# Optimization experiments

Measured on AMD Instinct MI355X. Metric: run time of the kernel, lower is better.

## Reference

```python
import jax, jax.numpy as jnp
import numpy as np
import math


def pos_enc_3d(h, w, d, c):
    # Faithful PositionalEncoding3D: channels = ceil(c/6)*2 (made even), sin/cos per axis.
    cpe = int(np.ceil(c / 6) * 2)
    if cpe % 2:
        cpe += 1
    inv_freq = 1.0 / (10000.0 ** (np.arange(0, cpe, 2, dtype=np.float32) / cpe))

    def axis_emb(n):
        s = np.arange(n, dtype=np.float32)[:, None] * inv_freq  # (n, cpe//2)
        return np.concatenate([np.sin(s), np.cos(s)], axis=-1)  # (n, cpe)

    ex = np.broadcast_to(axis_emb(h)[:, None, None, :], (h, w, d, cpe))
    ey = np.broadcast_to(axis_emb(w)[None, :, None, :], (h, w, d, cpe))
    ez = np.broadcast_to(axis_emb(d)[None, None, :, :], (h, w, d, cpe))
    emb = np.concatenate([ex, ey, ez], axis=-1)[..., :c]  # (h,w,d,c)
    return jnp.asarray(np.transpose(emb, (3, 0, 1, 2)))  # (c,h,w,d)


def conv3d(x, w, b):
    # x: (b,c,h,w,d), w: (o,i,3,3,3), padding=1
    y = jax.lax.conv_general_dilated(
        x, w, window_strides=(1, 1, 1), padding=[(1, 1)] * 3,
        dimension_numbers=('NCHWD', 'OIHWD', 'NCHWD'))
    return y + b[None, :, None, None, None]


def setup_inputs() -> dict:
    key = jax.random.key(0)
    ks = jax.random.split(key, 12)
    B, C, H, W, D = 2, 64, 16, 16, 16
    C8 = C // 8
    s_emb = 1.0 / math.sqrt(C)
    s_conv = 1.0 / math.sqrt(C * 27)
    return {
        'x': jax.random.normal(ks[0], (B, C, H, W, D), dtype=jnp.float32),
        'Wq': jax.random.normal(ks[1], (C, C), dtype=jnp.float32) * s_emb,
        'Wk': jax.random.normal(ks[2], (C, C), dtype=jnp.float32) * s_emb,
        'Wv': jax.random.normal(ks[3], (C, C), dtype=jnp.float32) * s_emb,
        'qw': jax.random.normal(ks[4], (C8, C, 3, 3, 3), dtype=jnp.float32) * s_conv,
        'qb': jax.random.normal(ks[5], (C8,), dtype=jnp.float32) * 0.01,
        'kw': jax.random.normal(ks[6], (C8, C, 3, 3, 3), dtype=jnp.float32) * s_conv,
        'kb': jax.random.normal(ks[7], (C8,), dtype=jnp.float32) * 0.01,
        'vw': jax.random.normal(ks[8], (C, C, 3, 3, 3), dtype=jnp.float32) * s_conv,
        'vb': jax.random.normal(ks[9], (C,), dtype=jnp.float32) * 0.01,
        'lam1': jax.random.normal(ks[10], (1,), dtype=jnp.float32) * 0.5,
        'lam2': jax.random.normal(ks[11], (1,), dtype=jnp.float32) * 0.5,
    }


def reference(x, Wq, Wk, Wv, qw, qb, kw, kb, vw, vb, lam1, lam2):
    b, c, h, w, d = x.shape
    n = h * w * d
    # NOTE: torch code does `x += pe` in-place inside SelfAttention, so the
    # PE-added x is also what GSA and the residual see.
    pe = pos_enc_3d(h, w, d, c)  # (c,h,w,d)
    x_pe = x + pe[None]

    # ---- SelfAttention (TSA) ----
    tok = x_pe.reshape(b, c, n).transpose(0, 2, 1)  # (b,n,c)
    Q = jnp.einsum('bnc,cd->bnd', tok, Wq)
    K = jnp.einsum('bnc,cd->bnd', tok, Wk)
    V = jnp.einsum('bnc,cd->bnd', tok, Wv)
    A = jax.nn.softmax(jnp.einsum('bic,bjc->bij', Q, K) / math.sqrt(c), axis=-1)
    tsa = jnp.einsum('bij,bjc->bic', A, V).transpose(0, 2, 1).reshape(b, c, h, w, d)

    # ---- GlobalSpatialAttention (GSA) ----
    M = conv3d(x_pe, qw, qb).reshape(b, c // 8, n)   # (b,c/8,n)
    Nk = conv3d(x_pe, kw, kb).reshape(b, c // 8, n)  # (b,c/8,n)
    Wv_ = conv3d(x_pe, vw, vb).reshape(b, c, n)      # (b,c,n)
    Bm = jax.nn.softmax(jnp.einsum('bci,bcj->bij', M, Nk), axis=-1)  # (b,n,n)
    gsa = jnp.einsum('bcj,bij->bci', Wv_, Bm).reshape(b, c, h, w, d)

    return lam1[0] * tsa + lam2[0] * gsa + x_pe
```

## Files before the change

### kernel.cpp

```cpp
#include <hip/hip_runtime.h>
#include <math.h>

#define BB 2
#define CC 64
#define NN 4096
#define CN (CC*NN)
#define NJ 8
#define NT ((NN/NJ)/64)

#define LOG2E 1.4426950408889634f
#define QSCALE 0.18033688011112042f
#define RESC_THR 8.0f

#define XT_ROWS 4097
#define WQKV_OFF (27*80*64)

typedef __attribute__((ext_vector_type(8))) short short8;
typedef __attribute__((ext_vector_type(4))) float float4v;
typedef unsigned short ushortT;

__device__ __forceinline__ ushortT f2bf(float x) {
    union { float f; unsigned u; } v; v.f = x;
    unsigned r = v.u + 0x7FFF + ((v.u >> 16) & 1);
    return (ushortT)(r >> 16);
}
__device__ __forceinline__ float bf2f(short s) {
    union { unsigned u; float f; } v;
    v.u = ((unsigned)(unsigned short)s) << 16;
    return v.f;
}
__device__ __forceinline__ unsigned pk2(float a, float b) {
    unsigned ua = __float_as_uint(a) + 0x8000u;
    unsigned ub = __float_as_uint(b) + 0x8000u;
    return __builtin_amdgcn_perm(ub, ua, 0x07060302);
}

__device__ __forceinline__ float pe_tab_val(int c, int pos) {
    int c2 = (c < 22) ? c : (c < 44) ? (c - 22) : (c - 44);
    int is_cos = (c2 >= 11);
    int k = c2 - (is_cos ? 11 : 0);
    float freq = exp2f(-1.2079738526863135f * (float)k);
    float arg = (float)pos * freq;
    return is_cos ? cosf(arg) : sinf(arg);
}

__global__ __launch_bounds__(256) void k_pre(const float* __restrict__ x,
                                             const float* __restrict__ qw,
                                             const float* __restrict__ kw,
                                             const float* __restrict__ vw,
                                             const float* __restrict__ Wq,
                                             const float* __restrict__ Wk,
                                             const float* __restrict__ Wv,
                                             float* __restrict__ xpe,
                                             ushortT* __restrict__ Xt,
                                             ushortT* __restrict__ Wr,
                                             ushortT* __restrict__ Qb,
                                             ushortT* __restrict__ Kb,
                                             ushortT* __restrict__ Vtb) {
    int blk = blockIdx.x, t = threadIdx.x;
    if (blk < 384) {
        __shared__ float sT[64][65];
        __shared__ float sPE[64][17];
        __shared__ ushortT sWt[64][72];
        __shared__ ushortT sVt[64][72];
        int mat = blk >> 7;
        int rest = blk & 127;
        int b = rest >> 6, pos0 = (rest & 63) * 64;

        #pragma unroll
        for (int k = 0; k < 4; k++) {
            int e = t + k * 256;
            int c = e >> 4, coord = e & 15;
            sPE[c][coord] = pe_tab_val(c, coord);
        }
        __syncthreads();

        int pin = t & 63, cg0 = t >> 6;
        #pragma unroll
        for (int pass = 0; pass < 16; pass++) {
            int c = pass * 4 + cg0;
            int pos = pos0 + pin;
            int coord = (c < 22) ? (pos >> 8) : (c < 44) ? ((pos >> 4) & 15) : (pos & 15);
            size_t gi = (size_t)(b * 64 + c) * NN + pos;
            float v = x[gi] + sPE[c][coord];
            if (mat == 0) xpe[gi] = v;
            sT[c][pin] = v;
        }
        {
            const float* Wm = (mat == 0) ? Wq : (mat == 1) ? Wk : Wv;
            float sc = (mat == 0) ? QSCALE : 1.f;
            #pragma unroll
            for (int p = 0; p < 4; p++) {
                int idx = t + p * 256;
                int c = idx >> 4, d4 = (idx & 15) * 4;
                float4 wv = *(const float4*)&Wm[c * 64 + d4];
                sWt[d4 + 0][c] = f2bf(wv.x * sc);
                sWt[d4 + 1][c] = f2bf(wv.y * sc);
                sWt[d4 + 2][c] = f2bf(wv.z * sc);
                sWt[d4 + 3][c] = f2bf(wv.w * sc);
            }
        }
        __syncthreads();

        if (mat == 0) {
            int po = t & 63, cg = t >> 6;
            #pragma unroll
            for (int half = 0; half < 2; half++) {
                int c0 = cg * 8 + half * 32;
                union { ushortT u[8]; short8 s; } pk_;
                #pragma unroll
                for (int e = 0; e < 8; e++) pk_.u[e] = f2bf(sT[c0 + e][po]);
                *(short8*)(Xt + ((size_t)b * XT_ROWS + pos0 + po + 1) * 64 + c0) = pk_.s;
            }
            if ((rest & 63) == 0 && t < 64)
                Xt[((size_t)b * XT_ROWS) * 64 + t] = 0;
        }

        int w = t >> 6, l = t & 63, lane15 = l & 15, q = l >> 4;
        int row = w * 16 + lane15;
        short8 a0, a1;
        {
            union { ushortT u[8]; short8 s; } t0, t1;
            #pragma unroll
            for (int e = 0; e < 8; e++) {
                t0.u[e] = f2bf(sT[q * 8 + e][row]);
                t1.u[e] = f2bf(sT[32 + q * 8 + e][row]);
            }
            a0 = t0.s; a1 = t1.s;
        }

        float4v acc[4];
        #pragma unroll
        for (int cg = 0; cg < 4; cg++) {
            const ushortT* wrow = &sWt[cg * 16 + lane15][0];
            short8 b0 = *(const short8*)(wrow + q * 8);
            short8 b1 = *(const short8*)(wrow + 32 + q * 8);
            float4v a = (float4v)0.f;
            a = __builtin_amdgcn_mfma_f32_16x16x32_bf16(a0, b0, a, 0, 0, 0);
            a = __builtin_amdgcn_mfma_f32_16x16x32_bf16(a1, b1, a, 0, 0, 0);
            acc[cg] = a;
        }
        if (mat < 2) {
            #pragma unroll
            for (int cg = 0; cg < 4; cg++)
                #pragma unroll
                for (int r = 0; r < 4; r++)
                    sVt[w * 16 + q * 4 + r][cg * 16 + lane15] = f2bf(acc[cg][r]);
            __syncthreads();
            ushortT* o = (mat == 0) ? Qb : Kb;
            int pl = t >> 2, sg = t & 3;
            short8 v0 = *(const short8*)&sVt[pl][sg * 16];
            short8 v1 = *(const short8*)&sVt[pl][sg * 16 + 8];
            size_t bq = ((size_t)(b * NN + pos0 + pl)) * 64 + sg * 16;
            *(short8*)(o + bq) = v0;
            *(short8*)(o + bq + 8) = v1;
        } else {
            #pragma unroll
            for (int cg = 0; cg < 4; cg++)
                #pragma unroll
                for (int r = 0; r < 4; r++)
                    sVt[cg * 16 + lane15][w * 16 + q * 4 + r] = f2bf(acc[cg][r]);
            __syncthreads();
            int c2 = t >> 2, seg = t & 3;
            short8 v0 = *(const short8*)&sVt[c2][seg * 16];
            short8 v1 = *(const short8*)&sVt[c2][seg * 16 + 8];
            size_t base = ((size_t)(b * 64 + c2)) * NN + pos0 + seg * 16;
            *(short8*)(Vtb + base) = v0;
            *(short8*)(Vtb + base + 8) = v1;
        }
    } else {
        int idx = (blk - 384) * 256 + t;
        if (idx < WQKV_OFF) {
            int ic = idx & 63;
            int oc = (idx >> 6) % 80;
            int tap = idx / 5120;
            float v;
            if (oc < 8)       v = qw[(oc * 64 + ic) * 27 + tap] * LOG2E;
            else if (oc < 16) v = kw[((oc - 8) * 64 + ic) * 27 + tap];
            else              v = vw[((oc - 16) * 64 + ic) * 27 + tap];
            Wr[idx] = f2bf(v);
        }
    }
}

template<int IS_TSA>
__device__ __forceinline__ void stage_load(short8* kst, short8* vst,
                                           const ushortT* __restrict__ Km,
                                           const ushortT* __restrict__ Vt,
                                           int b, int jb, int t) {
    if (IS_TSA) {
        #pragma unroll
        for (int ps = 0; ps < 2; ps++) {
            int idx = ps * 256 + t, j = idx >> 3, g = idx & 7;
            kst[ps] = *(const short8*)(Km + ((size_t)(b * NN + jb + j)) * 64 + g * 8);
        }
    } else {
        if (t < 64)
            kst[0] = *(const short8*)(Km + ((size_t)(b * NN + jb + t)) * 8);
    }
    #pragma unroll
    for (int ps = 0; ps < 2; ps++) {
        int idx = ps * 256 + t, c = idx >> 3, gj = idx & 7;
        vst[ps] = *(const short8*)(Vt + ((size_t)(b * 64 + c)) * NN + jb + gj * 8);
    }
}

template<int IS_TSA>
__device__ __forceinline__ void stage_write(const short8* kst, const short8* vst,
                                            ushortT* sK, ushortT* sV, int t) {
    if (IS_TSA) {
        #pragma unroll
        for (int ps = 0; ps < 2; ps++) {
            int idx = ps * 256 + t, j = idx >> 3, g = idx & 7;
            *(short8*)(sK + j * 64 + ((g ^ (j & 7)) * 8)) = kst[ps];
        }
    } else {
        if (t < 64)
            *(short8*)(sK + t * 64 + ((t & 7) * 8)) = kst[0];
    }
    #pragma unroll
    for (int ps = 0; ps < 2; ps++) {
        int idx = ps * 256 + t, c = idx >> 3, gj = idx & 7;
        *(short8*)(sV + c * 64 + ((gj ^ (c & 7)) * 8)) = vst[ps];
    }
}

template<int IS_TSA>
__device__ __forceinline__ void flash_body(int it, int jc, int b, int t,
                                           const ushortT* __restrict__ Qm,
                                           const ushortT* __restrict__ Km,
                                           const ushortT* __restrict__ Vt,
                                           float* __restrict__ pM,
                                           float* __restrict__ pL,
                                           ushortT* __restrict__ pAcc,
                                           ushortT* __restrict__ sKb,
                                           ushortT* __restrict__ sVb,
                                           ushortT* __restrict__ sPall) {
    constexpr int KCH = IS_TSA ? 2 : 1;
    constexpr int DQ  = IS_TSA ? 64 : 8;
    int w = t >> 6, l = t & 63;
    int lane15 = l & 15, q = l >> 4;
    int i0a = it * 128 + w * 16;
    ushortT* myP = sPall + w * (16 * 64);

    short8 qf[2][KCH];
    #pragma unroll
    for (int si = 0; si < 2; si++) {
        const ushortT* qrow = Qm + ((size_t)(b * NN + i0a + si * 64 + lane15)) * DQ;
        if (IS_TSA) {
            qf[si][0] = *(const short8*)(qrow + q * 8);
            qf[si][1] = *(const short8*)(qrow + 32 + q * 8);
        } else {
            short8 z = (short8)0;
            if (q == 0) z = *(const short8*)qrow;
            qf[si][0] = z;
        }
    }

    float m_run[2] = {-3e38f, -3e38f}, Lacc[2] = {0.f, 0.f};
    float4v O[2][4];
    #pragma unroll
    for (int si = 0; si < 2; si++)
        #pragma unroll
        for (int cs = 0; cs < 4; cs++) O[si][cs] = (float4v)0.f;

    const int jbase0 = jc * (NN / NJ);

    short8 kst[2], vst[2];
    stage_load<IS_TSA>(kst, vst, Km, Vt, b, jbase0, t);
    stage_write<IS_TSA>(kst, vst, sKb, sVb, t);
    __syncthreads();

    for (int jt = 0; jt < NT; jt++) {
        int cur = jt & 1;
        ushortT* cK = sKb + cur * 4096;
        ushortT* cV = sVb + cur * 4096;
        bool more = (jt + 1 < NT);

        if (more) stage_load<IS_TSA>(kst, vst, Km, Vt, b, jbase0 + (jt + 1) * 64, t);

        short8 kf[4][KCH];
        #pragma unroll
        for (int sub = 0; sub < 4; sub++) {
            int jr = sub * 16 + lane15;
            if (IS_TSA) {
                kf[sub][0] = *(const short8*)(cK + jr * 64 + (((0 * 4 + q) ^ (lane15 & 7)) * 8));
                kf[sub][1] = *(const short8*)(cK + jr * 64 + (((1 * 4 + q) ^ (lane15 & 7)) * 8));
            } else {
                short8 z = (short8)0;
                if (q == 0) z = *(const short8*)(cK + jr * 64 + ((lane15 & 7) * 8));
                kf[sub][0] = z;
            }
        }

        float4v s[2][4];
        #pragma unroll
        for (int si = 0; si < 2; si++)
            #pragma unroll
            for (int sub = 0; sub < 4; sub++) {
                float4v acc = (float4v)0.f;
                #pragma unroll
                for (int kc = 0; kc < KCH; kc++)
                    acc = __builtin_amdgcn_mfma_f32_16x16x32_bf16(kf[sub][kc], qf[si][kc], acc, 0, 0, 0);
                s[si][sub] = acc;
            }

        short8 va[4], vbf[4];
        #pragma unroll
        for (int sub = 0; sub < 4; sub++) {
            int cr = sub * 16 + lane15;
            va[sub]  = *(const short8*)(cV + cr * 64 + ((q ^ (lane15 & 7)) * 8));
            vbf[sub] = *(const short8*)(cV + cr * 64 + (((4 + q) ^ (lane15 & 7)) * 8));
        }

        #pragma unroll
        for (int si = 0; si < 2; si++) {
            float tmax = fmaxf(fmaxf(fmaxf(s[si][0][0], s[si][0][1]), fmaxf(s[si][0][2], s[si][0][3])),
                               fmaxf(fmaxf(s[si][1][0], s[si][1][1]), fmaxf(s[si][1][2], s[si][1][3])));
            float tmax2 = fmaxf(fmaxf(fmaxf(s[si][2][0], s[si][2][1]), fmaxf(s[si][2][2], s[si][2][3])),
                                fmaxf(fmaxf(s[si][3][0], s[si][3][1]), fmaxf(s[si][3][2], s[si][3][3])));
            tmax = fmaxf(tmax, tmax2);
            tmax = fmaxf(tmax, __shfl_xor(tmax, 16));
            tmax = fmaxf(tmax, __shfl_xor(tmax, 32));

            if (!__all(tmax <= m_run[si] + RESC_THR)) {
                float mnew = fmaxf(m_run[si], tmax);
                float corr = exp2f(m_run[si] - mnew);
                Lacc[si] *= corr;
                float c0 = __shfl(corr, q * 4 + 0);
                float c1 = __shfl(corr, q * 4 + 1);
                float c2 = __shfl(corr, q * 4 + 2);
                float c3 = __shfl(corr, q * 4 + 3);
                #pragma unroll
                for (int cs = 0; cs < 4; cs++) {
                    O[si][cs][0] *= c0; O[si][cs][1] *= c1;
                    O[si][cs][2] *= c2; O[si][cs][3] *= c3;
                }
                m_run[si] = mnew;
            }
            float mcur = m_run[si];

            #pragma unroll
            for (int sub = 0; sub < 4; sub++) {
                float p0 = exp2f(s[si][sub][0] - mcur);
                float p1 = exp2f(s[si][sub][1] - mcur);
                float p2 = exp2f(s[si][sub][2] - mcur);
                float p3 = exp2f(s[si][sub][3] - mcur);
                Lacc[si] += (p0 + p1) + (p2 + p3);
                unsigned lo = pk2(p0, p1), hi = pk2(p2, p3);
                int g = sub * 2 + (q >> 1);
                unsigned* wp = (unsigned*)(myP + lane15 * 64 + ((g ^ (lane15 & 7)) * 8) + (q & 1) * 4);
                wp[0] = lo; wp[1] = hi;
            }

            short8 pf0 = *(const short8*)(myP + lane15 * 64 + (((0 * 4 + q) ^ (lane15 & 7)) * 8));
            short8 pf1 = *(const short8*)(myP + lane15 * 64 + (((1 * 4 + q) ^ (lane15 & 7)) * 8));

            #pragma unroll
            for (int sub = 0; sub < 4; sub++) {
                O[si][sub] = __builtin_amdgcn_mfma_f32_16x16x32_bf16(pf0, va[sub], O[si][sub], 0, 0, 0);
                O[si][sub] = __builtin_amdgcn_mfma_f32_16x16x32_bf16(pf1, vbf[sub], O[si][sub], 0, 0, 0);
            }
        }

        if (more) {
            stage_write<IS_TSA>(kst, vst, sKb + (cur ^ 1) * 4096, sVb + (cur ^ 1) * 4096, t);
            __syncthreads();
        }
    }

    #pragma unroll
    for (int si = 0; si < 2; si++) {
        size_t base = (size_t)(b * NJ + jc) * NN + i0a + si * 64;
        float Ls = Lacc[si];
        Ls += __shfl_xor(Ls, 16);
        Ls += __shfl_xor(Ls, 32);
        if (q == 0) {
            pL[base + lane15] = Ls;
            pM[base + lane15] = m_run[si];
        }
        #pragma unroll
        for (int cs = 0; cs < 4; cs++) {
            int g = cs * 2 + (lane15 >> 3);
            #pragma unroll
            for (int r = 0; r < 4; r++) {
                int rr = q * 4 + r;
                myP[rr * 64 + ((g ^ (rr & 7)) * 8) + (lane15 & 7)] = f2bf(O[si][cs][r]);
            }
        }
        int rrow = l >> 2, rs2 = (l & 3) * 2;
        short8 ov0 = *(const short8*)(myP + rrow * 64 + ((rs2 ^ (rrow & 7)) * 8));
        short8 ov1 = *(const short8*)(myP + rrow * 64 + (((rs2 + 1) ^ (rrow & 7)) * 8));
        size_t gb = (base + rrow) * 64 + (l & 3) * 16;
        *(short8*)(pAcc + gb) = ov0;
        *(short8*)(pAcc + gb + 8) = ov1;
    }
}

__device__ __forceinline__ void reduce_set(const float* __restrict__ pM,
                                           const float* __restrict__ pL,
                                           const ushortT* __restrict__ pAcc,
                                           int b, int n, int seg, float* v) {
    float mv[NJ], M = -3e38f;
    #pragma unroll
    for (int jcc = 0; jcc < NJ; jcc++) {
        mv[jcc] = pM[(size_t)(b * NJ + jcc) * NN + n];
        M = fmaxf(M, mv[jcc]);
    }
    float L = 0.f;
    #pragma unroll
    for (int e = 0; e < 8; e++) v[e] = 0.f;
    #pragma unroll
    for (int jcc = 0; jcc < NJ; jcc++) {
        size_t rb = (size_t)(b * NJ + jcc) * NN + n;
        float wgt = exp2f(mv[jcc] - M);
        L += pL[rb] * wgt;
        short8 x0 = *(const short8*)(pAcc + rb * 64 + seg * 8);
        #pragma unroll
        for (int e = 0; e < 8; e++) v[e] += wgt * bf2f(x0[e]);
    }
    float invL = 1.f / L;
    #pragma unroll
    for (int e = 0; e < 8; e++) v[e] *= invL;
}

__global__ __launch_bounds__(256, 3) void k_tsacv(const ushortT* __restrict__ Qb,
                                                  const ushortT* __restrict__ Kb,
                                                  const ushortT* __restrict__ Vtb,
                                                  const ushortT* __restrict__ Xt,
                                                  const ushortT* __restrict__ Wr,
                                                  const float* __restrict__ qb,
                                                  const float* __restrict__ kb,
                                                  const float* __restrict__ vb,
                                                  ushortT* __restrict__ Mt,
                                                  ushortT* __restrict__ Nt,
                                                  ushortT* __restrict__ Wvt,
                                                  float* __restrict__ pMt, float* __restrict__ pLt,
                                                  ushortT* __restrict__ pAccT) {
    __shared__ ushortT sm[20480];
    int bx = blockIdx.x, t = threadIdx.x;
    if (bx >= 128) {
        int fb = bx - 128;
        int it = fb & 31, jc = (fb >> 5) & 7, b = fb >> 8;
        flash_body<1>(it, jc, b, t, Qb, Kb, Vtb, pMt, pLt, pAccT,
                      sm, sm + 8192, sm + 16384);
    } else {
        int cv = bx;
        int tile = cv & 63, b = cv >> 6;
        int w = t >> 6, l = t & 63, lane15 = l & 15, q = l >> 4;
        int pos0 = tile * 64 + w * 16;
        const ushortT* xb = Xt + (size_t)b * XT_ROWS * 64;
        int pos = pos0 + lane15;
        int dz = pos & 15, wy = (pos >> 4) & 15, hx = pos >> 8;

        ushortT* sW = sm;

        float4v accA[5], accB[5];
        #pragma unroll
        for (int o = 0; o < 5; o++) { accA[o] = (float4v)0.f; accB[o] = (float4v)0.f; }

        short8 ws[3];
        auto ldW = [&](int tap) {
            #pragma unroll
            for (int c3 = 0; c3 < 3; c3++) {
                int idx = t + c3 * 256;
                if (idx < 640)
                    ws[c3] = *(const short8*)(Wr + (size_t)tap * 5120 + idx * 8);
            }
        };
        auto wrW = [&](ushortT* buf) {
            #pragma unroll
            for (int c3 = 0; c3 < 3; c3++) {
                int idx = t + c3 * 256;
                if (idx < 640) {
                    int row = idx >> 3, g = idx & 7;
                    *(short8*)(buf + row * 64 + ((g ^ (row & 7)) * 8)) = ws[c3];
                }
            }
        };
        short8 xc0, xc1, xn0, xn1;
        auto ldX = [&](int tap, short8& o0, short8& o1) {
            int dh = tap / 9 - 1, dw = (tap / 3) % 3 - 1, dd = tap % 3 - 1;
            int shift = dh * 256 + dw * 16 + dd;
            bool ok = ((unsigned)(hx + dh) < 16u) &&
                      ((unsigned)(wy + dw) < 16u) &&
                      ((unsigned)(dz + dd) < 16u);
            int row = ok ? (pos + shift + 1) : 0;
            const ushortT* xrow = xb + (size_t)row * 64 + q * 8;
            o0 = *(const short8*)xrow;
            o1 = *(const short8*)(xrow + 32);
        };

        ldW(0);
        ldX(0, xc0, xc1);
        wrW(sW);
        __syncthreads();

        #pragma unroll
        for (int tap = 0; tap < 27; tap++) {
            ushortT* cW = sW + (tap & 1) * 5120;
            bool more = (tap + 1 < 27);

            if (more) { ldW(tap + 1); ldX(tap + 1, xn0, xn1); }

            #pragma unroll
            for (int o = 0; o < 5; o++) {
                int wr2 = o * 16 + lane15;
                short8 a0 = *(const short8*)(cW + wr2 * 64 + ((q ^ (lane15 & 7)) * 8));
                short8 a1 = *(const short8*)(cW + wr2 * 64 + (((4 + q) ^ (lane15 & 7)) * 8));
                accA[o] = __builtin_amdgcn_mfma_f32_16x16x32_bf16(a0, xc0, accA[o], 0, 0, 0);
                accB[o] = __builtin_amdgcn_mfma_f32_16x16x32_bf16(a1, xc1, accB[o], 0, 0, 0);
            }

            if (more) wrW(sW + ((tap + 1) & 1) * 5120);
            __syncthreads();
            xc0 = xn0; xc1 = xn1;
        }

        #pragma unroll
        for (int o = 0; o < 5; o++) {
            float4v accT = accA[o] + accB[o];
            if (o == 0) {
                #pragma unroll
                for (int r = 0; r < 4; r++) {
                    int ol = q * 4 + r;
                    float v = accT[r];
                    if (ol < 8)
                        Mt[((size_t)(b * NN + pos)) * 8 + ol] = f2bf(v + qb[ol] * LOG2E);
                    else
                        Nt[((size_t)(b * NN + pos)) * 8 + (ol - 8)] = f2bf(v + kb[ol - 8]);
                }
            } else {
                #pragma unroll
                for (int r = 0; r < 4; r++) {
                    int oc = (o - 1) * 16 + q * 4 + r;
                    Wvt[((size_t)(b * 64 + oc)) * NN + pos] = f2bf(accT[r] + vb[oc]);
                }
            }
        }
    }
}

__global__ __launch_bounds__(256, 3) void k_gsa(const ushortT* __restrict__ Mtb,
                                                const ushortT* __restrict__ Ntb,
                                                const ushortT* __restrict__ Wvtb,
                                                float* __restrict__ pMg, float* __restrict__ pLg,
                                                ushortT* __restrict__ pAccG,
                                                const float* __restrict__ pMt,
                                                const float* __restrict__ pLt,
                                                const ushortT* __restrict__ pAccT,
                                                const float* __restrict__ xpe,
                                                const float* __restrict__ lam1,
                                                float* __restrict__ out) {
    __shared__ ushortT sm[20480];
    int bx = blockIdx.x, t = threadIdx.x;
    if (bx < 512) {
        int it = bx & 31, jc = (bx >> 5) & 7, b = bx >> 8;
        flash_body<0>(it, jc, b, t, Mtb, Ntb, Wvtb, pMg, pLg, pAccG,
                      sm, sm + 8192, sm + 16384);
    } else {
        int rb = bx - 512;
        int b = rb >> 7, n0 = (rb & 127) * 32;
        float (*sT_)[65] = (float(*)[65])sm;
        int pp = t >> 3, seg = t & 7, n = n0 + pp;

        float vt[8];
        reduce_set(pMt, pLt, pAccT, b, n, seg, vt);
        #pragma unroll
        for (int e = 0; e < 8; e++) sT_[pp][seg * 8 + e] = vt[e];
        __syncthreads();

        int c = t >> 2, ns = (t & 3) * 8;
        float la1 = lam1[0];
        size_t ob = ((size_t)(b * 64 + c)) * NN + n0 + ns;
        const float* xp = xpe + ob;
        #pragma unroll
        for (int j = 0; j < 8; j += 4) {
            float4 ov;
            ov.x = la1 * sT_[ns + j + 0][c] + xp[j + 0];
            ov.y = la1 * sT_[ns + j + 1][c] + xp[j + 1];
            ov.z = la1 * sT_[ns + j + 2][c] + xp[j + 2];
            ov.w = la1 * sT_[ns + j + 3][c] + xp[j + 3];
            *(float4*)(out + ob + j) = ov;
        }
    }
}

__global__ __launch_bounds__(256) void k_reduce_g(const float* __restrict__ pMg,
                                                  const float* __restrict__ pLg,
                                                  const ushortT* __restrict__ pAccG,
                                                  const float* __restrict__ lam2,
                                                  float* __restrict__ out) {
    __shared__ float sG[32][65];
    int t = threadIdx.x;
    int b = blockIdx.y;
    int n0 = blockIdx.x * 32;
    int pp = t >> 3, seg = t & 7;
    int n = n0 + pp;

    float vg[8];
    reduce_set(pMg, pLg, pAccG, b, n, seg, vg);
    #pragma unroll
    for (int e = 0; e < 8; e++) sG[pp][seg * 8 + e] = vg[e];
    __syncthreads();

    int c = t >> 2, ns = (t & 3) * 8;
    float la2 = lam2[0];
    size_t ob = ((size_t)(b * 64 + c)) * NN + n0 + ns;
    #pragma unroll
    for (int j = 0; j < 8; j += 4) {
        float4 cur = *(const float4*)(out + ob + j);
        cur.x += la2 * sG[ns + j + 0][c];
        cur.y += la2 * sG[ns + j + 1][c];
        cur.z += la2 * sG[ns + j + 2][c];
        cur.w += la2 * sG[ns + j + 3][c];
        *(float4*)(out + ob + j) = cur;
    }
}

extern "C" void kernel_launch(void* const* d_in, const int* in_sizes, int n_in,
                              void* d_out, int out_size, void* d_ws, size_t ws_size,
                              hipStream_t stream) {
    const float* x    = (const float*)d_in[0];
    const float* Wq   = (const float*)d_in[1];
    const float* Wk   = (const float*)d_in[2];
    const float* Wv   = (const float*)d_in[3];
    const float* qw   = (const float*)d_in[4];
    const float* qb   = (const float*)d_in[5];
    const float* kw   = (const float*)d_in[6];
    const float* kb   = (const float*)d_in[7];
    const float* vw   = (const float*)d_in[8];
    const float* vb   = (const float*)d_in[9];
    const float* lam1 = (const float*)d_in[10];
    const float* lam2 = (const float*)d_in[11];
    float* out = (float*)d_out;

    char* W = (char*)d_ws;
    float*   xpe   = (float*)(W);
    ushortT* Qb    = (ushortT*)(W + (2u << 20));
    ushortT* Kb    = (ushortT*)(W + (3u << 20));
    ushortT* Vtb   = (ushortT*)(W + (4u << 20));
    ushortT* Mtb   = (ushortT*)(W + (5u << 20));
    ushortT* Ntb   = (ushortT*)(W + (5u << 20) + (1u << 17));
    ushortT* Wvtb  = (ushortT*)(W + (5u << 20) + (2u << 17));
    ushortT* Xt    = (ushortT*)(W + (6u << 20) + (2u << 17));
    ushortT* Wr    = (ushortT*)(W + (7u << 20) + (1u << 19));
    float*   pLt   = (float*)(W + (8u << 20));
    float*   pLg   = (float*)(W + (8u << 20) + (1u << 18));
    float*   pMt   = (float*)(W + (8u << 20) + (2u << 18));
    float*   pMg   = (float*)(W + (8u << 20) + (3u << 18));
    ushortT* pAccT = (ushortT*)(W + (9u << 20));
    ushortT* pAccG = (ushortT*)(W + (17u << 20));

    k_pre<<<dim3(384 + WQKV_OFF / 256), dim3(256), 0, stream>>>(
        x, qw, kw, vw, Wq, Wk, Wv, xpe, Xt, Wr, Qb, Kb, Vtb);
    k_tsacv<<<dim3(128 + 32 * NJ * BB), dim3(256), 0, stream>>>(
        Qb, Kb, Vtb, Xt, Wr, qb, kb, vb, Mtb, Ntb, Wvtb, pMt, pLt, pAccT);
    k_gsa<<<dim3(512 + 256), dim3(256), 0, stream>>>(
        Mtb, Ntb, Wvtb, pMg, pLg, pAccG, pMt, pLt, pAccT, xpe, lam1, out);
    k_reduce_g<<<dim3(NN / 32, BB), dim3(256), 0, stream>>>(
        pMg, pLg, pAccG, lam2, out);
}
```

Before: 133.4 us.

## Double block size to 512 threads with one query tile per wave

Flash-attention blocks in both the TSA and GSA kernels now use 8 waves of 512 threads, each owning a single 16-row query tile, instead of 4 waves each handling two tiles. Per-thread register state (O accumulators, running max and sum, Q fragments) is halved, and K/V staging is spread across more threads. The conv and reduce paths are remapped to the wider blocks, with half as many conv blocks. The intent is more waves per CU for latency hiding, at the cost of a tighter register budget under launch_bounds(512,4), a larger shared-memory footprint and more barrier participants.

Measured after the change: 133.2 us. No clear change (-0.1%).

```diff
diff --git a/kernel.cpp b/kernel.cpp
--- a/kernel.cpp
+++ b/kernel.cpp
@@ -189,40 +189,28 @@
                                            const ushortT* __restrict__ Vt,
                                            int b, int jb, int t) {
     if (IS_TSA) {
-        #pragma unroll
-        for (int ps = 0; ps < 2; ps++) {
-            int idx = ps * 256 + t, j = idx >> 3, g = idx & 7;
-            kst[ps] = *(const short8*)(Km + ((size_t)(b * NN + jb + j)) * 64 + g * 8);
-        }
+        int j = t >> 3, g = t & 7;
+        kst[0] = *(const short8*)(Km + ((size_t)(b * NN + jb + j)) * 64 + g * 8);
     } else {
         if (t < 64)
             kst[0] = *(const short8*)(Km + ((size_t)(b * NN + jb + t)) * 8);
     }
-    #pragma unroll
-    for (int ps = 0; ps < 2; ps++) {
-        int idx = ps * 256 + t, c = idx >> 3, gj = idx & 7;
-        vst[ps] = *(const short8*)(Vt + ((size_t)(b * 64 + c)) * NN + jb + gj * 8);
-    }
+    int c = t >> 3, gj = t & 7;
+    vst[0] = *(const short8*)(Vt + ((size_t)(b * 64 + c)) * NN + jb + gj * 8);
 }
 
 template<int IS_TSA>
 __device__ __forceinline__ void stage_write(const short8* kst, const short8* vst,
                                             ushortT* sK, ushortT* sV, int t) {
     if (IS_TSA) {
-        #pragma unroll
-        for (int ps = 0; ps < 2; ps++) {
-            int idx = ps * 256 + t, j = idx >> 3, g = idx & 7;
-            *(short8*)(sK + j * 64 + ((g ^ (j & 7)) * 8)) = kst[ps];
-        }
+        int j = t >> 3, g = t & 7;
+        *(short8*)(sK + j * 64 + ((g ^ (j & 7)) * 8)) = kst[0];
     } else {
         if (t < 64)
             *(short8*)(sK + t * 64 + ((t & 7) * 8)) = kst[0];
     }
-    #pragma unroll
-    for (int ps = 0; ps < 2; ps++) {
-        int idx = ps * 256 + t, c = idx >> 3, gj = idx & 7;
-        *(short8*)(sV + c * 64 + ((gj ^ (c & 7)) * 8)) = vst[ps];
-    }
+    int c = t >> 3, gj = t & 7;
+    *(short8*)(sV + c * 64 + ((gj ^ (c & 7)) * 8)) = vst[0];
 }
 
 template<int IS_TSA>
@@ -240,33 +228,30 @@
     constexpr int DQ  = IS_TSA ? 64 : 8;
     int w = t >> 6, l = t & 63;
     int lane15 = l & 15, q = l >> 4;
-    int i0a = it * 128 + w * 16;
+    int i0a = it * 128 + (w & 3) * 16 + (w >> 2) * 64;
     ushortT* myP = sPall + w * (16 * 64);
 
-    short8 qf[2][KCH];
-    #pragma unroll
-    for (int si = 0; si < 2; si++) {
-        const ushortT* qrow = Qm + ((size_t)(b * NN + i0a + si * 64 + lane15)) * DQ;
+    short8 qf[KCH];
+    {
+        const ushortT* qrow = Qm + ((size_t)(b * NN + i0a + lane15)) * DQ;
         if (IS_TSA) {
-            qf[si][0] = *(const short8*)(qrow + q * 8);
-            qf[si][1] = *(const short8*)(qrow + 32 + q * 8);
+            qf[0] = *(const short8*)(qrow + q * 8);
+            qf[1] = *(const short8*)(qrow + 32 + q * 8);
         } else {
             short8 z = (short8)0;
             if (q == 0) z = *(const short8*)qrow;
-            qf[si][0] = z;
-        }
-    }
-
-    float m_run[2] = {-3e38f, -3e38f}, Lacc[2] = {0.f, 0.f};
-    float4v O[2][4];
+            qf[0] = z;
+        }
+    }
+
+    float m_run = -3e38f, Lacc = 0.f;
+    float4v O[4];
     #pragma unroll
-    for (int si = 0; si < 2; si++)
-        #pragma unroll
-        for (int cs = 0; cs < 4; cs++) O[si][cs] = (float4v)0.f;
+    for (int cs = 0; cs < 4; cs++) O[cs] = (float4v)0.f;
 
     const int jbase0 = jc * (NN / NJ);
 
-    short8 kst[2], vst[2];
+    short8 kst[1], vst[1];
     stage_load<IS_TSA>(kst, vst, Km, Vt, b, jbase0, t);
     stage_write<IS_TSA>(kst, vst, sKb, sVb, t);
     __syncthreads();
@@ -293,17 +278,15 @@
             }
         }
 
-        float4v s[2][4];
-        #pragma unroll
-        for (int si = 0; si < 2; si++)
-            #pragma unroll
-            for (int sub = 0; sub < 4; sub++) {
-                float4v acc = (float4v)0.f;
-                #pragma unroll
-                for (int kc = 0; kc < KCH; kc++)
-                    acc = __builtin_amdgcn_mfma_f32_16x16x32_bf16(kf[sub][kc], qf[si][kc], acc, 0, 0, 0);
-                s[si][sub] = acc;
-            }
+        float4v s[4];
+        #pragma unroll
+        for (int sub = 0; sub < 4; sub++) {
+            float4v acc = (float4v)0.f;
+            #pragma unroll
+            for (int kc = 0; kc < KCH; kc++)
+                acc = __builtin_amdgcn_mfma_f32_16x16x32_bf16(kf[sub][kc], qf[kc], acc, 0, 0, 0);
+            s[sub] = acc;
+        }
 
         short8 va[4], vbf[4];
         #pragma unroll
@@ -313,40 +296,39 @@
             vbf[sub] = *(const short8*)(cV + cr * 64 + (((4 + q) ^ (lane15 & 7)) * 8));
         }
 
-        #pragma unroll
-        for (int si = 0; si < 2; si++) {
-            float tmax = fmaxf(fmaxf(fmaxf(s[si][0][0], s[si][0][1]), fmaxf(s[si][0][2], s[si][0][3])),
-                               fmaxf(fmaxf(s[si][1][0], s[si][1][1]), fmaxf(s[si][1][2], s[si][1][3])));
-            float tmax2 = fmaxf(fmaxf(fmaxf(s[si][2][0], s[si][2][1]), fmaxf(s[si][2][2], s[si][2][3])),
-                                fmaxf(fmaxf(s[si][3][0], s[si][3][1]), fmaxf(s[si][3][2], s[si][3][3])));
+        {
+            float tmax = fmaxf(fmaxf(fmaxf(s[0][0], s[0][1]), fmaxf(s[0][2], s[0][3])),
+                               fmaxf(fmaxf(s[1][0], s[1][1]), fmaxf(s[1][2], s[1][3])));
+            float tmax2 = fmaxf(fmaxf(fmaxf(s[2][0], s[2][1]), fmaxf(s[2][2], s[2][3])),
+                                fmaxf(fmaxf(s[3][0], s[3][1]), fmaxf(s[3][2], s[3][3])));
             tmax = fmaxf(tmax, tmax2);
             tmax = fmaxf(tmax, __shfl_xor(tmax, 16));
             tmax = fmaxf(tmax, __shfl_xor(tmax, 32));
 
-            if (!__all(tmax <= m_run[si] + RESC_THR)) {
-                float mnew = fmaxf(m_run[si], tmax);
-                float corr = exp2f(m_run[si] - mnew);
-                Lacc[si] *= corr;
+            if (!__all(tmax <= m_run + RESC_THR)) {
+                float mnew = fmaxf(m_run, tmax);
+                float corr = exp2f(m_run - mnew);
+                Lacc *= corr;
                 float c0 = __shfl(corr, q * 4 + 0);
                 float c1 = __shfl(corr, q * 4 + 1);
                 float c2 = __shfl(corr, q * 4 + 2);
                 float c3 = __shfl(corr, q * 4 + 3);
                 #pragma unroll
                 for (int cs = 0; cs < 4; cs++) {
-                    O[si][cs][0] *= c0; O[si][cs][1] *= c1;
-                    O[si][cs][2] *= c2; O[si][cs][3] *= c3;
+                    O[cs][0] *= c0; O[cs][1] *= c1;
+                    O[cs][2] *= c2; O[cs][3] *= c3;
                 }
-                m_run[si] = mnew;
-            }
-            float mcur = m_run[si];
+                m_run = mnew;
+            }
+            float mcur = m_run;
 
             #pragma unroll
             for (int sub = 0; sub < 4; sub++) {
-                float p0 = exp2f(s[si][sub][0] - mcur);
-                float p1 = exp2f(s[si][sub][1] - mcur);
-                float p2 = exp2f(s[si][sub][2] - mcur);
-                float p3 = exp2f(s[si][sub][3] - mcur);
-                Lacc[si] += (p0 + p1) + (p2 + p3);
+                float p0 = exp2f(s[sub][0] - mcur);
+                float p1 = exp2f(s[sub][1] - mcur);
+                float p2 = exp2f(s[sub][2] - mcur);
+                float p3 = exp2f(s[sub][3] - mcur);
+                Lacc += (p0 + p1) + (p2 + p3);
                 unsigned lo = pk2(p0, p1), hi = pk2(p2, p3);
                 int g = sub * 2 + (q >> 1);
                 unsigned* wp = (unsigned*)(myP + lane15 * 64 + ((g ^ (lane15 & 7)) * 8) + (q & 1) * 4);
@@ -358,8 +340,8 @@
 
             #pragma unroll
             for (int sub = 0; sub < 4; sub++) {
-                O[si][sub] = __builtin_amdgcn_mfma_f32_16x16x32_bf16(pf0, va[sub], O[si][sub], 0, 0, 0);
-                O[si][sub] = __builtin_amdgcn_mfma_f32_16x16x32_bf16(pf1, vbf[sub], O[si][sub], 0, 0, 0);
+                O[sub] = __builtin_amdgcn_mfma_f32_16x16x32_bf16(pf0, va[sub], O[sub], 0, 0, 0);
+                O[sub] = __builtin_amdgcn_mfma_f32_16x16x32_bf16(pf1, vbf[sub], O[sub], 0, 0, 0);
             }
         }
 
@@ -369,15 +351,14 @@
         }
     }
 
-    #pragma unroll
-    for (int si = 0; si < 2; si++) {
-        size_t base = (size_t)(b * NJ + jc) * NN + i0a + si * 64;
-        float Ls = Lacc[si];
+    {
+        size_t base = (size_t)(b * NJ + jc) * NN + i0a;
+        float Ls = Lacc;
         Ls += __shfl_xor(Ls, 16);
         Ls += __shfl_xor(Ls, 32);
         if (q == 0) {
             pL[base + lane15] = Ls;
-            pM[base + lane15] = m_run[si];
+            pM[base + lane15] = m_run;
         }
         #pragma unroll
         for (int cs = 0; cs < 4; cs++) {
@@ -385,7 +366,7 @@
             #pragma unroll
             for (int r = 0; r < 4; r++) {
                 int rr = q * 4 + r;
-                myP[rr * 64 + ((g ^ (rr & 7)) * 8) + (lane15 & 7)] = f2bf(O[si][cs][r]);
+                myP[rr * 64 + ((g ^ (rr & 7)) * 8) + (lane15 & 7)] = f2bf(O[cs][r]);
             }
         }
         int rrow = l >> 2, rs2 = (l & 3) * 2;
@@ -424,7 +405,7 @@
     for (int e = 0; e < 8; e++) v[e] *= invL;
 }
 
-__global__ __launch_bounds__(256, 3) void k_tsacv(const ushortT* __restrict__ Qb,
+__global__ __launch_bounds__(512, 4) void k_tsacv(const ushortT* __restrict__ Qb,
                                                   const ushortT* __restrict__ Kb,
                                                   const ushortT* __restrict__ Vtb,
                                                   const ushortT* __restrict__ Xt,
@@ -437,18 +418,18 @@
                                                   ushortT* __restrict__ Wvt,
                                                   float* __restrict__ pMt, float* __restrict__ pLt,
                                                   ushortT* __restrict__ pAccT) {
-    __shared__ ushortT sm[20480];
+    __shared__ ushortT sm[24576];
     int bx = blockIdx.x, t = threadIdx.x;
-    if (bx >= 128) {
-        int fb = bx - 128;
+    if (bx >= 64) {
+        int fb = bx - 64;
         int it = fb & 31, jc = (fb >> 5) & 7, b = fb >> 8;
         flash_body<1>(it, jc, b, t, Qb, Kb, Vtb, pMt, pLt, pAccT,
                       sm, sm + 8192, sm + 16384);
     } else {
         int cv = bx;
-        int tile = cv & 63, b = cv >> 6;
+        int tile = cv & 31, b = cv >> 5;
         int w = t >> 6, l = t & 63, lane15 = l & 15, q = l >> 4;
-        int pos0 = tile * 64 + w * 16;
+        int pos0 = tile * 128 + w * 16;
         const ushortT* xb = Xt + (size_t)b * XT_ROWS * 64;
         int pos = pos0 + lane15;
         int dz = pos & 15, wy = (pos >> 4) & 15, hx = pos >> 8;
@@ -459,19 +440,19 @@
         #pragma unroll
         for (int o = 0; o < 5; o++) { accA[o] = (float4v)0.f; accB[o] = (float4v)0.f; }
 
-        short8 ws[3];
+        short8 ws[2];
         auto ldW = [&](int tap) {
             #pragma unroll
-            for (int c3 = 0; c3 < 3; c3++) {
-                int idx = t + c3 * 256;
+            for (int c3 = 0; c3 < 2; c3++) {
+                int idx = t + c3 * 512;
                 if (idx < 640)
                     ws[c3] = *(const short8*)(Wr + (size_t)tap * 5120 + idx * 8);
             }
         };
         auto wrW = [&](ushortT* buf) {
             #pragma unroll
-            for (int c3 = 0; c3 < 3; c3++) {
-                int idx = t + c3 * 256;
+            for (int c3 = 0; c3 < 2; c3++) {
+                int idx = t + c3 * 512;
                 if (idx < 640) {
                     int row = idx >> 3, g = idx & 7;
                     *(short8*)(buf + row * 64 + ((g ^ (row & 7)) * 8)) = ws[c3];
@@ -541,7 +522,7 @@
     }
 }
 
-__global__ __launch_bounds__(256, 3) void k_gsa(const ushortT* __restrict__ Mtb,
+__global__ __launch_bounds__(512, 4) void k_gsa(const ushortT* __restrict__ Mtb,
                                                 const ushortT* __restrict__ Ntb,
                                                 const ushortT* __restrict__ Wvtb,
                                                 float* __restrict__ pMg, float* __restrict__ pLg,
@@ -552,7 +533,7 @@
                                                 const float* __restrict__ xpe,
                                                 const float* __restrict__ lam1,
                                                 float* __restrict__ out) {
-    __shared__ ushortT sm[20480];
+    __shared__ ushortT sm[24576];
     int bx = blockIdx.x, t = threadIdx.x;
     if (bx < 512) {
         int it = bx & 31, jc = (bx >> 5) & 7, b = bx >> 8;
@@ -562,27 +543,25 @@
         int rb = bx - 512;
         int b = rb >> 7, n0 = (rb & 127) * 32;
         float (*sT_)[65] = (float(*)[65])sm;
-        int pp = t >> 3, seg = t & 7, n = n0 + pp;
-
-        float vt[8];
-        reduce_set(pMt, pLt, pAccT, b, n, seg, vt);
-        #pragma unroll
-        for (int e = 0; e < 8; e++) sT_[pp][seg * 8 + e] = vt[e];
+        if (t < 256) {
+            int pp = t >> 3, seg = t & 7, n = n0 + pp;
+            float vt[8];
+            reduce_set(pMt, pLt, pAccT, b, n, seg, vt);
+            #pragma unroll
+            for (int e = 0; e < 8; e++) sT_[pp][seg * 8 + e] = vt[e];
+        }
         __syncthreads();
 
-        int c = t >> 2, ns = (t & 3) * 8;
+        int c = t >> 3, ns = (t & 7) * 4;
         float la1 = lam1[0];
         size_t ob = ((size_t)(b * 64 + c)) * NN + n0 + ns;
         const float* xp = xpe + ob;
-        #pragma unroll
-        for (int j = 0; j < 8; j += 4) {
-            float4 ov;
-            ov.x = la1 * sT_[ns + j + 0][c] + xp[j + 0];
-            ov.y = la1 * sT_[ns + j + 1][c] + xp[j + 1];
-            ov.z = la1 * sT_[ns + j + 2][c] + xp[j + 2];
-            ov.w = la1 * sT_[ns + j + 3][c] + xp[j + 3];
-            *(float4*)(out + ob + j) = ov;
-        }
+        float4 ov;
+        ov.x = la1 * sT_[ns + 0][c] + xp[0];
+        ov.y = la1 * sT_[ns + 1][c] + xp[1];
+        ov.z = la1 * sT_[ns + 2][c] + xp[2];
+        ov.w = la1 * sT_[ns + 3][c] + xp[3];
+        *(float4*)(out + ob) = ov;
     }
 }
 
@@ -654,9 +633,9 @@
 
     k_pre<<<dim3(384 + WQKV_OFF / 256), dim3(256), 0, stream>>>(
         x, qw, kw, vw, Wq, Wk, Wv, xpe, Xt, Wr, Qb, Kb, Vtb);
-    k_tsacv<<<dim3(128 + 32 * NJ * BB), dim3(256), 0, stream>>>(
+    k_tsacv<<<dim3(64 + 32 * NJ * BB), dim3(512), 0, stream>>>(
         Qb, Kb, Vtb, Xt, Wr, qb, kb, vb, Mtb, Ntb, Wvtb, pMt, pLt, pAccT);
-    k_gsa<<<dim3(512 + 256), dim3(256), 0, stream>>>(
+    k_gsa<<<dim3(512 + 256), dim3(512), 0, stream>>>(
         Mtb, Ntb, Wvtb, pMg, pLg, pAccG, pMt, pLt, pAccT, xpe, lam1, out);
     k_reduce_g<<<dim3(NN / 32, BB), dim3(256), 0, stream>>>(
         pMg, pLg, pAccG, lam2, out);
```
